# Performance work log

Hardware: AMD Instinct MI355X
Metric: run time of the kernel (lower is better)

## Reference

```python
import jax, jax.numpy as jnp
import numpy as np

H = 512
W = 512


def setup_inputs() -> dict:
    key = jax.random.key(0)
    k1, k2 = jax.random.split(key)
    B, P, C = 8, 30000, 64
    pillar_features = jax.random.normal(k1, (B, P, C), dtype=jnp.float32)
    pillar_coords = jax.random.randint(k2, (B, P, 2), 0, 512, dtype=jnp.int32)
    return {"pillar_features": pillar_features, "pillar_coords": pillar_coords}


def _scatter_one(feat, coords):
    # feat: (P, C), coords: (P, 2) as [gx, gy]
    gx = coords[:, 0]
    gy = coords[:, 1]
    valid = (gx >= 0) & (gx < W) & (gy >= 0) & (gy < H)
    # invalid pillars -> out-of-range flat index, dropped by mode='drop'
    flat = jnp.where(valid, gy * W + gx, H * W)
    bev = jnp.zeros((H * W, feat.shape[1]), dtype=feat.dtype)
    bev = bev.at[flat].set(feat, mode="drop")
    # (H*W, C) -> (C, H, W)
    return bev.reshape(H, W, -1).transpose(2, 0, 1)


def reference(pillar_features, pillar_coords):
    return jax.vmap(_scatter_one)(pillar_features, pillar_coords)
```

## Files before the change

### kernel.cpp

```cpp
#include <hip/hip_runtime.h>

#define BEV_H 512
#define BEV_W 512
#define BEV_HW (BEV_H * BEV_W)
#define NB 8
#define NP 30000
#define NC 64

__global__ void scatter_winner_kernel(const int* __restrict__ coords,
                                      int* __restrict__ winner) {
    int idx = blockIdx.x * blockDim.x + threadIdx.x;
    if (idx >= NB * NP) return;
    int b = idx / NP;
    int p = idx - b * NP;
    int2 c2 = ((const int2*)coords)[idx];
    int gx = c2.x;
    int gy = c2.y;
    if (gx >= 0 && gx < BEV_W && gy >= 0 && gy < BEV_H) {
        atomicMax(&winner[b * BEV_HW + gy * BEV_W + gx], p);
    }
}

__global__ void gather_out_kernel(const float* __restrict__ feat,
                                  const int* __restrict__ winner,
                                  float* __restrict__ out) {
    int bc = blockIdx.y;
    int b  = bc >> 6;
    int c  = bc & (NC - 1);
    int cell = (blockIdx.x * blockDim.x + threadIdx.x) << 2;

    const int4 w4 = *(const int4*)(winner + (size_t)b * BEV_HW + cell);
    const float* fb = feat + (size_t)b * NP * NC + c;

    float4 v;
    v.x = (w4.x >= 0) ? fb[(size_t)w4.x * NC] : 0.0f;
    v.y = (w4.y >= 0) ? fb[(size_t)w4.y * NC] : 0.0f;
    v.z = (w4.z >= 0) ? fb[(size_t)w4.z * NC] : 0.0f;
    v.w = (w4.w >= 0) ? fb[(size_t)w4.w * NC] : 0.0f;

    *(float4*)(out + (size_t)bc * BEV_HW + cell) = v;
}

extern "C" void kernel_launch(void* const* d_in, const int* in_sizes, int n_in,
                              void* d_out, int out_size, void* d_ws, size_t ws_size,
                              hipStream_t stream) {
    const float* feat   = (const float*)d_in[0];
    const int*   coords = (const int*)d_in[1];
    float*       out    = (float*)d_out;
    int*         winner = (int*)d_ws;

    hipMemsetAsync(winner, 0xFF, (size_t)NB * BEV_HW * sizeof(int), stream);

    {
        int total = NB * NP;
        int block = 256;
        int grid  = (total + block - 1) / block;
        scatter_winner_kernel<<<grid, block, 0, stream>>>(coords, winner);
    }

    {
        dim3 block(256, 1, 1);
        dim3 grid(BEV_HW / (4 * 256), NB * NC, 1);
        gather_out_kernel<<<grid, block, 0, stream>>>(feat, winner, out);
    }
}
```

Before: 596.2 us.

## Gather full feature rows per cell instead of per-channel strided loads

Each thread now handles one BEV cell for all 64 channels. It reads the winner index once and loads the whole contiguous feature row with vector loads, then writes each channel plane. This is meant to remove the repeated winner reads and the scattered single-float gathers from the feature tensor. The cost is higher register use per thread and scalar rather than float4 stores.

```diff
diff --git a/kernel.cpp b/kernel.cpp
--- a/kernel.cpp
+++ b/kernel.cpp
@@ -24,21 +24,29 @@
 __global__ void gather_out_kernel(const float* __restrict__ feat,
                                   const int* __restrict__ winner,
                                   float* __restrict__ out) {
-    int bc = blockIdx.y;
-    int b  = bc >> 6;
-    int c  = bc & (NC - 1);
-    int cell = (blockIdx.x * blockDim.x + threadIdx.x) << 2;
+    int b = blockIdx.y;
+    int cell = blockIdx.x * blockDim.x + threadIdx.x;
 
-    const int4 w4 = *(const int4*)(winner + (size_t)b * BEV_HW + cell);
-    const float* fb = feat + (size_t)b * NP * NC + c;
+    int w = winner[b * BEV_HW + cell];
 
-    float4 v;
-    v.x = (w4.x >= 0) ? fb[(size_t)w4.x * NC] : 0.0f;
-    v.y = (w4.y >= 0) ? fb[(size_t)w4.y * NC] : 0.0f;
-    v.z = (w4.z >= 0) ? fb[(size_t)w4.z * NC] : 0.0f;
-    v.w = (w4.w >= 0) ? fb[(size_t)w4.w * NC] : 0.0f;
+    float4 r[16];
+    if (w >= 0) {
+        const float4* row = (const float4*)(feat + ((size_t)b * NP + w) * NC);
+        #pragma unroll
+        for (int j = 0; j < 16; ++j) r[j] = row[j];
+    } else {
+        #pragma unroll
+        for (int j = 0; j < 16; ++j) r[j] = make_float4(0.f, 0.f, 0.f, 0.f);
+    }
 
-    *(float4*)(out + (size_t)bc * BEV_HW + cell) = v;
+    float* o = out + (size_t)b * NC * BEV_HW + cell;
+    #pragma unroll
+    for (int j = 0; j < 16; ++j) {
+        o[(size_t)(4 * j + 0) * BEV_HW] = r[j].x;
+        o[(size_t)(4 * j + 1) * BEV_HW] = r[j].y;
+        o[(size_t)(4 * j + 2) * BEV_HW] = r[j].z;
+        o[(size_t)(4 * j + 3) * BEV_HW] = r[j].w;
+    }
 }
 
 extern "C" void kernel_launch(void* const* d_in, const int* in_sizes, int n_in,
@@ -60,7 +68,7 @@
 
     {
         dim3 block(256, 1, 1);
-        dim3 grid(BEV_HW / (4 * 256), NB * NC, 1);
+        dim3 grid(BEV_HW / 256, NB, 1);
         gather_out_kernel<<<grid, block, 0, stream>>>(feat, winner, out);
     }
 }
```

After: 609.2 us. 1.02x slower.
